# Kernel optimization log

Measured on AMD Instinct MI355X. Metric: run time of the kernel, lower is better.

Reference implementation:

```python
import jax, jax.numpy as jnp
import numpy as np
import math

N_HEADS = 8
D_E = 64


def setup_inputs() -> dict:
    key = jax.random.key(0)
    k1, k2, k3 = jax.random.split(key, 3)
    B, C, L = 4, 512, 2048
    x = jax.random.normal(k1, (B, C, L), dtype=jnp.float32)
    # 1x1-conv (channel-mixing) projection shared by Q and K (the original
    # uses query_conv for both Q and K).
    W_q = jax.random.normal(k2, (N_HEADS * D_E, C), dtype=jnp.float32) * 0.02
    b_q = jax.random.normal(k3, (N_HEADS * D_E,), dtype=jnp.float32) * 0.02
    return {"x": x, "W_q": W_q, "b_q": b_q}


def reference(x, W_q, b_q):
    B, C, L = x.shape
    H, d_e = N_HEADS, D_E
    # 1x1 conv over channels: (B, H*d_e, L)
    qk = jnp.einsum('oc,bcl->bol', W_q, x) + b_q[None, :, None]
    # (B, H, L, d_e); K == Q per the original (both use query_conv)
    Q = qk.reshape(B, H, d_e, L).transpose(0, 1, 3, 2)
    K = Q
    scores = jnp.einsum('bhqd,bhkd->bhqk', Q, K) / math.sqrt(d_e)
    # causal mask: positions k > q masked to -inf (triu(diagonal=1) masked)
    causal = jnp.arange(L)[None, :] <= jnp.arange(L)[:, None]  # (L, L)
    scores = jnp.where(causal[None, None], scores, -jnp.inf)
    A = jax.nn.softmax(scores, axis=-1)  # (B, H, L, L)
    # values are the raw input sequence, (B, L, C)
    V = x.transpose(0, 2, 1)
    H_att = jnp.einsum('bhqk,bkc->bhqc', A, V)  # (B, H, L, C)
    out = H_att + V[:, None]                      # residual add per head
    # -> (B, H*C, L)
    return out.transpose(0, 1, 3, 2).reshape(B, H * C, L)
```

## Files before the change

### kernel.cpp

```cpp
#include <hip/hip_runtime.h>
#include <hip/hip_bf16.h>

#define B_ 4
#define C_ 512
#define L_ 2048
#define H_ 8
#define E_ 64
#define QSCALE 0.4246609f
#define NUNITS 1024

typedef __attribute__((ext_vector_type(8))) short bf16x8;
typedef __attribute__((ext_vector_type(4))) float f32x4;
typedef __attribute__((ext_vector_type(4))) unsigned short u16x4;

static __device__ __forceinline__ unsigned short f2bf(float f) {
    union { float f; unsigned u; } v; v.f = f;
    unsigned r = v.u + 0x7FFFu + ((v.u >> 16) & 1u);
    return (unsigned short)(r >> 16);
}

#define LBAR() do { asm volatile("s_waitcnt lgkmcnt(0)" ::: "memory"); \
                    __builtin_amdgcn_s_barrier(); } while (0)

__global__ __launch_bounds__(256) void prep_kernel(const float* __restrict__ x,
                                                   unsigned short* __restrict__ xb,
                                                   unsigned short* __restrict__ xt) {
    const int lt = blockIdx.x, ct = blockIdx.y, b = blockIdx.z;
    const int l0 = lt * 64, c0 = ct * 64;
    const int t = threadIdx.x;
    __shared__ unsigned short T[64 * 72];

    const int cl = t >> 2, lo = (t & 3) * 16;
    const float* src = x + ((size_t)(b * C_ + c0 + cl)) * L_ + l0 + lo;
    unsigned short u[16];
    #pragma unroll
    for (int j = 0; j < 16; j += 4) {
        float4 v = *reinterpret_cast<const float4*>(src + j);
        u[j] = f2bf(v.x); u[j + 1] = f2bf(v.y); u[j + 2] = f2bf(v.z); u[j + 3] = f2bf(v.w);
    }
    unsigned short* xbp = xb + ((size_t)(b * C_ + c0 + cl)) * L_ + l0 + lo;
    reinterpret_cast<uint4*>(xbp)[0] = reinterpret_cast<uint4*>(u)[0];
    reinterpret_cast<uint4*>(xbp)[1] = reinterpret_cast<uint4*>(u)[1];
    reinterpret_cast<uint4*>(&T[cl * 72 + lo])[0] = reinterpret_cast<uint4*>(u)[0];
    reinterpret_cast<uint4*>(&T[cl * 72 + lo + 8])[0] = reinterpret_cast<uint4*>(u)[1];
    __syncthreads();
    const int ll = t >> 2, co = (t & 3) * 16;
    unsigned short v16[16];
    #pragma unroll
    for (int j = 0; j < 16; ++j) v16[j] = T[(co + j) * 72 + ll];
    unsigned short* xtp = xt + ((size_t)b * L_ + l0 + ll) * C_ + c0 + co;
    reinterpret_cast<uint4*>(xtp)[0] = reinterpret_cast<uint4*>(v16)[0];
    reinterpret_cast<uint4*>(xtp)[1] = reinterpret_cast<uint4*>(v16)[1];
}

__global__ __launch_bounds__(256) void wcast_kernel(const float* __restrict__ W,
                                                    unsigned short* __restrict__ Wb) {
    const int i = blockIdx.x * 256 + threadIdx.x;
    float4 v = reinterpret_cast<const float4*>(W)[i];
    union { unsigned short u[4]; unsigned long long ll; } o;
    o.u[0] = f2bf(v.x); o.u[1] = f2bf(v.y); o.u[2] = f2bf(v.z); o.u[3] = f2bf(v.w);
    reinterpret_cast<unsigned long long*>(Wb)[i] = o.ll;
}

__global__ __launch_bounds__(256) void proj_kernel(const unsigned short* __restrict__ Wb,
                                                   const float* __restrict__ bq,
                                                   const unsigned short* __restrict__ xt,
                                                   unsigned short* __restrict__ qb) {
    const int lt = blockIdx.x, h = blockIdx.y, b = blockIdx.z;
    const int tid = threadIdx.x, w = tid >> 6, lane = tid & 63;
    const int lr = lane & 15, lg = lane >> 4;
    const int l = lt * 64 + w * 16 + lr;
    const int o0 = h * 64;

    f32x4 acc[4] = {};
    const unsigned short* xrow = xt + ((size_t)b * L_ + l) * C_;
    for (int ks = 0; ks < 16; ++ks) {
        bf16x8 bf = *reinterpret_cast<const bf16x8*>(xrow + ks * 32 + lg * 8);
        #pragma unroll
        for (int mt = 0; mt < 4; ++mt) {
            bf16x8 af = *reinterpret_cast<const bf16x8*>(Wb + (size_t)(o0 + mt * 16 + lr) * C_ + ks * 32 + lg * 8);
            acc[mt] = __builtin_amdgcn_mfma_f32_16x16x32_bf16(af, bf, acc[mt], 0, 0, 0);
        }
    }
    const int bh = b * H_ + h;
    unsigned short* qrow = qb + ((size_t)bh * L_ + l) * 64;
    #pragma unroll
    for (int mt = 0; mt < 4; ++mt) {
        const int e0 = mt * 16 + lg * 4;
        const float4 bb = *reinterpret_cast<const float4*>(bq + o0 + e0);
        union { unsigned short u[4]; unsigned long long ll; } o;
        o.u[0] = f2bf((acc[mt][0] + bb.x) * QSCALE);
        o.u[1] = f2bf((acc[mt][1] + bb.y) * QSCALE);
        o.u[2] = f2bf((acc[mt][2] + bb.z) * QSCALE);
        o.u[3] = f2bf((acc[mt][3] + bb.w) * QSCALE);
        *reinterpret_cast<unsigned long long*>(qrow + e0) = o.ll;
    }
}

#define LDVB(BK, KOFF)                                                                  \
    {                                                                                   \
        _Pragma("unroll")                                                               \
        for (int ct = 0; ct < 4; ++ct)                                                  \
            pvv[BK][ct] = *reinterpret_cast<const bf16x8*>(                             \
                Vbase + (size_t)(c0w + ct * 16 + lr) * L_ + (KOFF) + lg * 8);           \
    }

#define PV_STEP(CUR, NXT, S_)                                                           \
    {                                                                                   \
        const int s_ = (S_);                                                            \
        if (s_ + 1 < ksmax) LDVB(NXT, k0 + (s_ + 1) * 32)                               \
        bf16x8 pa[4];                                                                   \
        _Pragma("unroll")                                                               \
        for (int mt = 0; mt < 4; ++mt) {                                                \
            const int row = mt * 16 + lr;                                               \
            const int g2 = (s_ * 4 + lg) ^ (lr & 7);                                    \
            pa[mt] = *reinterpret_cast<const bf16x8*>(&P[row * 512 + (g2 << 3)]);       \
        }                                                                               \
        __builtin_amdgcn_s_setprio(1);                                                  \
        _Pragma("unroll")                                                               \
        for (int mt = 0; mt < 4; ++mt)                                                  \
            _Pragma("unroll")                                                           \
            for (int ct = 0; ct < 4; ++ct)                                              \
                acc[mt][ct] = __builtin_amdgcn_mfma_f32_16x16x32_bf16(                  \
                    pa[mt], pvv[CUR][ct], acc[mt][ct], 0, 0, 0);                        \
        __builtin_amdgcn_s_setprio(0);                                                  \
    }

__global__ __launch_bounds__(512, 2) void pv_kernel(const unsigned short* __restrict__ qb,
                                                    const unsigned short* __restrict__ xb,
                                                    float* __restrict__ out,
                                                    int* __restrict__ counter) {
    const int tid = threadIdx.x, w = tid >> 6, lane = tid & 63;
    const int lr = lane & 15, lg = lane >> 4;
    const int c0w = w * 64;

    __shared__ unsigned short Qt[64 * 64];
    __shared__ unsigned short P[64 * 512];
    __shared__ float rsT[64][8];
    __shared__ int s_u;

    for (;;) {
        __syncthreads();
        if (tid == 0) s_u = atomicAdd(counter, 1);
        __syncthreads();
        const int u = s_u;
        if (u >= NUNITS) return;

        const int qt = 31 - (u >> 5);
        const int rr = u & 31;
        const int b = rr >> 3, h = rr & 7;
        const int q0 = qt * 64, qlim = q0 + 63;
        const int nkt = (q0 >> 9) + 1;
        const int bh = b * H_ + h;
        const unsigned short* Qbase = qb + (size_t)bh * L_ * 64;
        const unsigned short* Vbase = xb + (size_t)b * C_ * L_;

        {
            const int r = tid >> 3, g = tid & 7;
            bf16x8 v = *reinterpret_cast<const bf16x8*>(Qbase + (size_t)(q0 + r) * 64 + g * 8);
            *reinterpret_cast<bf16x8*>(&Qt[r * 64 + ((g ^ (r & 7)) << 3)]) = v;
        }

        bf16x8 pvv[2][4];
        f32x4 acc[4][4] = {};
        float rs[4] = {0.f, 0.f, 0.f, 0.f};

        LBAR();

        #pragma unroll 1
        for (int kt = 0; kt < nkt; ++kt) {
            const int k0 = kt * 512;
            const int ksmax = min(16, ((qlim - k0) >> 5) + 1);
            const int kw0 = k0 + w * 64;

            if (kw0 <= qlim) {
                bf16x8 kb[4][2];
                #pragma unroll
                for (int ksub = 0; ksub < 4; ++ksub) {
                    const size_t krow = (size_t)(kw0 + ksub * 16 + lr) * 64;
                    kb[ksub][0] = *reinterpret_cast<const bf16x8*>(Qbase + krow + lg * 8);
                    kb[ksub][1] = *reinterpret_cast<const bf16x8*>(Qbase + krow + 32 + lg * 8);
                }
                LDVB(0, k0)
                #pragma unroll
                for (int nt = 0; nt < 4; ++nt) {
                    const int qrow = nt * 16 + lr;
                    bf16x8 aq0 = *reinterpret_cast<const bf16x8*>(&Qt[qrow * 64 + ((lg ^ (lr & 7)) << 3)]);
                    bf16x8 aq1 = *reinterpret_cast<const bf16x8*>(&Qt[qrow * 64 + (((4 + lg) ^ (lr & 7)) << 3)]);
                    const int q = q0 + qrow;
                    #pragma unroll
                    for (int ksub = 0; ksub < 4; ++ksub) {
                        f32x4 z = {};
                        z = __builtin_amdgcn_mfma_f32_16x16x32_bf16(kb[ksub][0], aq0, z, 0, 0, 0);
                        z = __builtin_amdgcn_mfma_f32_16x16x32_bf16(kb[ksub][1], aq1, z, 0, 0, 0);
                        const int kbase = kw0 + ksub * 16 + lg * 4;
                        const float p0 = (kbase + 0 <= q) ? exp2f(z[0]) : 0.f;
                        const float p1 = (kbase + 1 <= q) ? exp2f(z[1]) : 0.f;
                        const float p2 = (kbase + 2 <= q) ? exp2f(z[2]) : 0.f;
                        const float p3 = (kbase + 3 <= q) ? exp2f(z[3]) : 0.f;
                        rs[nt] += (p0 + p1) + (p2 + p3);
                        unsigned r01, r23;
                        asm("v_cvt_pk_bf16_f32 %0, %1, %2" : "=v"(r01) : "v"(p0), "v"(p1));
                        asm("v_cvt_pk_bf16_f32 %0, %1, %2" : "=v"(r23) : "v"(p2), "v"(p3));
                        const int kl = w * 64 + ksub * 16 + lg * 4;
                        const int gg = (kl >> 3) ^ (qrow & 7);
                        const unsigned long long pk = ((unsigned long long)r23 << 32) | r01;
                        *reinterpret_cast<unsigned long long*>(&P[qrow * 512 + (gg << 3) + (kl & 7)]) = pk;
                    }
                }
            } else {
                LDVB(0, k0)
            }
            LBAR();

            #pragma unroll 1
            for (int s = 0; s < ksmax; s += 2) {
                PV_STEP(0, 1, s)
                PV_STEP(1, 0, s + 1)
            }
            LBAR();
        }

        #pragma unroll
        for (int nt = 0; nt < 4; ++nt) {
            float t0 = __shfl_xor(rs[nt], 16); rs[nt] += t0;
            float t1 = __shfl_xor(rs[nt], 32); rs[nt] += t1;
        }
        if (lg == 0) {
            #pragma unroll
            for (int nt = 0; nt < 4; ++nt) rsT[nt * 16 + lr][w] = rs[nt];
        }
        LBAR();

        const unsigned short* xres = xb + (size_t)b * C_ * L_;
        float* ob = out + (size_t)bh * C_ * L_;
        #pragma unroll
        for (int mt = 0; mt < 4; ++mt) {
            f32x4 li;
            #pragma unroll
            for (int r = 0; r < 4; ++r) {
                const f32x4 s0 = *reinterpret_cast<const f32x4*>(&rsT[mt * 16 + lg * 4 + r][0]);
                const f32x4 s1 = *reinterpret_cast<const f32x4*>(&rsT[mt * 16 + lg * 4 + r][4]);
                li[r] = 1.f / (((s0[0] + s0[1]) + (s0[2] + s0[3])) + ((s1[0] + s1[1]) + (s1[2] + s1[3])));
            }
            const int lbase = q0 + mt * 16 + lg * 4;
            #pragma unroll
            for (int ct = 0; ct < 4; ++ct) {
                const int c = c0w + ct * 16 + lr;
                const u16x4 rv = __builtin_nontemporal_load(
                    reinterpret_cast<const u16x4*>(xres + (size_t)c * L_ + lbase));
                f32x4 o;
                o[0] = acc[mt][ct][0] * li[0] + __uint_as_float((unsigned)rv[0] << 16);
                o[1] = acc[mt][ct][1] * li[1] + __uint_as_float((unsigned)rv[1] << 16);
                o[2] = acc[mt][ct][2] * li[2] + __uint_as_float((unsigned)rv[2] << 16);
                o[3] = acc[mt][ct][3] * li[3] + __uint_as_float((unsigned)rv[3] << 16);
                __builtin_nontemporal_store(o, reinterpret_cast<f32x4*>(ob + (size_t)c * L_ + lbase));
            }
        }
    }
}

extern "C" void kernel_launch(void* const* d_in, const int* in_sizes, int n_in,
                              void* d_out, int out_size, void* d_ws, size_t ws_size,
                              hipStream_t stream) {
    const float* x  = (const float*)d_in[0];
    const float* Wq = (const float*)d_in[1];
    const float* bq = (const float*)d_in[2];
    float* out = (float*)d_out;

    unsigned short* xb   = (unsigned short*)d_ws;
    unsigned short* xt   = xb + (size_t)B_ * C_ * L_;
    unsigned short* qbuf = xt + (size_t)B_ * L_ * C_;
    unsigned short* Wb   = qbuf + (size_t)B_ * H_ * L_ * E_;
    int* counter = (int*)(Wb + (size_t)H_ * E_ * C_);

    (void)hipMemsetAsync(counter, 0, 4, stream);
    prep_kernel<<<dim3(32, 8, 4), 256, 0, stream>>>(x, xb, xt);
    wcast_kernel<<<dim3(256), 256, 0, stream>>>(Wq, Wb);
    proj_kernel<<<dim3(32, 8, 4), 256, 0, stream>>>(Wb, bq, xt, qbuf);
    pv_kernel<<<dim3(512), 512, 0, stream>>>(qbuf, xb, out, counter);
}
```

Measured before the change: 256.0 us.

## Pin blocks to per-batch work queues and deepen V prefetch to two steps

```diff
diff --git a/kernel.cpp b/kernel.cpp
--- a/kernel.cpp
+++ b/kernel.cpp
@@ -7,7 +7,7 @@
 #define H_ 8
 #define E_ 64
 #define QSCALE 0.4246609f
-#define NUNITS 1024
+#define NUNITS_B 256
 
 typedef __attribute__((ext_vector_type(8))) short bf16x8;
 typedef __attribute__((ext_vector_type(4))) float f32x4;
@@ -108,7 +108,7 @@
 #define PV_STEP(CUR, NXT, S_)                                                           \
     {                                                                                   \
         const int s_ = (S_);                                                            \
-        if (s_ + 1 < ksmax) LDVB(NXT, k0 + (s_ + 1) * 32)                               \
+        if (s_ + 2 < ksmax) LDVB(NXT, k0 + (s_ + 2) * 32)                               \
         bf16x8 pa[4];                                                                   \
         _Pragma("unroll")                                                               \
         for (int mt = 0; mt < 4; ++mt) {                                                \
@@ -129,31 +129,33 @@
 __global__ __launch_bounds__(512, 2) void pv_kernel(const unsigned short* __restrict__ qb,
                                                     const unsigned short* __restrict__ xb,
                                                     float* __restrict__ out,
-                                                    int* __restrict__ counter) {
+                                                    int* __restrict__ counters) {
     const int tid = threadIdx.x, w = tid >> 6, lane = tid & 63;
     const int lr = lane & 15, lg = lane >> 4;
     const int c0w = w * 64;
+    const int myb = (blockIdx.x & 7) >> 1;
 
     __shared__ unsigned short Qt[64 * 64];
     __shared__ unsigned short P[64 * 512];
     __shared__ float rsT[64][8];
     __shared__ int s_u;
 
+    const int b = myb;
+    const unsigned short* Vbase = xb + (size_t)b * C_ * L_;
+
     for (;;) {
         __syncthreads();
-        if (tid == 0) s_u = atomicAdd(counter, 1);
+        if (tid == 0) s_u = atomicAdd(counters + myb, 1);
         __syncthreads();
         const int u = s_u;
-        if (u >= NUNITS) return;
-
-        const int qt = 31 - (u >> 5);
-        const int rr = u & 31;
-        const int b = rr >> 3, h = rr & 7;
+        if (u >= NUNITS_B) return;
+
+        const int qt = 31 - (u >> 3);
+        const int h = u & 7;
         const int q0 = qt * 64, qlim = q0 + 63;
         const int nkt = (q0 >> 9) + 1;
         const int bh = b * H_ + h;
         const unsigned short* Qbase = qb + (size_t)bh * L_ * 64;
-        const unsigned short* Vbase = xb + (size_t)b * C_ * L_;
 
         {
             const int r = tid >> 3, g = tid & 7;
@@ -161,7 +163,7 @@
             *reinterpret_cast<bf16x8*>(&Qt[r * 64 + ((g ^ (r & 7)) << 3)]) = v;
         }
 
-        bf16x8 pvv[2][4];
+        bf16x8 pvv[4][4];
         f32x4 acc[4][4] = {};
         float rs[4] = {0.f, 0.f, 0.f, 0.f};
 
@@ -182,6 +184,7 @@
                     kb[ksub][1] = *reinterpret_cast<const bf16x8*>(Qbase + krow + 32 + lg * 8);
                 }
                 LDVB(0, k0)
+                LDVB(1, k0 + 32)
                 #pragma unroll
                 for (int nt = 0; nt < 4; ++nt) {
                     const int qrow = nt * 16 + lr;
@@ -210,13 +213,21 @@
                 }
             } else {
                 LDVB(0, k0)
+                LDVB(1, k0 + 32)
             }
             LBAR();
 
+            int s = 0;
             #pragma unroll 1
-            for (int s = 0; s < ksmax; s += 2) {
-                PV_STEP(0, 1, s)
-                PV_STEP(1, 0, s + 1)
+            for (; s + 4 <= ksmax; s += 4) {
+                PV_STEP(0, 2, s)
+                PV_STEP(1, 3, s + 1)
+                PV_STEP(2, 0, s + 2)
+                PV_STEP(3, 1, s + 3)
+            }
+            if (s < ksmax) {
+                PV_STEP(0, 2, s)
+                PV_STEP(1, 3, s + 1)
             }
             LBAR();
         }
@@ -272,11 +283,11 @@
     unsigned short* xt   = xb + (size_t)B_ * C_ * L_;
     unsigned short* qbuf = xt + (size_t)B_ * L_ * C_;
     unsigned short* Wb   = qbuf + (size_t)B_ * H_ * L_ * E_;
-    int* counter = (int*)(Wb + (size_t)H_ * E_ * C_);
-
-    (void)hipMemsetAsync(counter, 0, 4, stream);
+    int* counters = (int*)(Wb + (size_t)H_ * E_ * C_);
+
+    (void)hipMemsetAsync(counters, 0, 16, stream);
     prep_kernel<<<dim3(32, 8, 4), 256, 0, stream>>>(x, xb, xt);
     wcast_kernel<<<dim3(256), 256, 0, stream>>>(Wq, Wb);
     proj_kernel<<<dim3(32, 8, 4), 256, 0, stream>>>(Wb, bq, xt, qbuf);
-    pv_kernel<<<dim3(512), 512, 0, stream>>>(qbuf, xb, out, counter);
-}
+    pv_kernel<<<dim3(512), 512, 0, stream>>>(qbuf, xb, out, counters);
+}
```

Result: no change. 251.8 us (-1.6%).
